# Performance work log

Measured on AMD Instinct MI355X. Metric: run time of the kernel, lower is better.

The kernel has to match this reference:

```python
import jax, jax.numpy as jnp
import numpy as np

HIDDEN = 2048
N_HEADS = 16
N_KV_HEADS = 4
HEAD_DIM = HIDDEN // N_HEADS  # 128
ROPE_THETA = 10000.0
BATCH = 2
SEQ = 2048


def setup_inputs() -> dict:
    key = jax.random.key(0)
    k1, k2, k3, k4, k5 = jax.random.split(key, 5)
    s = 0.02
    return {
        "hidden_states": jax.random.normal(k1, (BATCH, SEQ, HIDDEN), dtype=jnp.float32),
        "attention_mask": jnp.zeros((BATCH, 1, 1, SEQ), dtype=jnp.float32),
        "Wq": jax.random.normal(k2, (HIDDEN, N_HEADS * HEAD_DIM), dtype=jnp.float32) * s,
        "Wk": jax.random.normal(k3, (HIDDEN, N_KV_HEADS * HEAD_DIM), dtype=jnp.float32) * s,
        "Wv": jax.random.normal(k4, (HIDDEN, N_KV_HEADS * HEAD_DIM), dtype=jnp.float32) * s,
        "Wo": jax.random.normal(k5, (N_HEADS * HEAD_DIM, HIDDEN), dtype=jnp.float32) * s,
    }


def _rope_cos_sin(seq_len, dtype):
    inv_freq = 1.0 / (ROPE_THETA ** (jnp.arange(0, HEAD_DIM, 2, dtype=jnp.float32) / HEAD_DIM))
    t = jnp.arange(seq_len, dtype=jnp.float32)
    freqs = t[:, None] * inv_freq[None, :]            # [S, D/2]
    emb = jnp.concatenate([freqs, freqs], axis=-1)    # [S, D]
    cos = jnp.cos(emb)[None, None, :, :].astype(dtype)  # [1,1,S,D]
    sin = jnp.sin(emb)[None, None, :, :].astype(dtype)
    return cos, sin


def _apply_rope(x, cos, sin):
    # x: [B,H,S,D]; faithful to torch code: rotated = cat((-x[...,1::2], x[...,::2]), -1)
    x1 = x[..., ::2]
    x2 = x[..., 1::2]
    rotated = jnp.concatenate([-x2, x1], axis=-1)
    return x * cos + rotated * sin


def reference(hidden_states, attention_mask, Wq, Wk, Wv, Wo):
    B, S, _ = hidden_states.shape
    scale = HEAD_DIM ** -0.5

    q = (hidden_states @ Wq).reshape(B, S, N_HEADS, HEAD_DIM).transpose(0, 2, 1, 3)      # [B,H,S,D]
    k = (hidden_states @ Wk).reshape(B, S, N_KV_HEADS, HEAD_DIM).transpose(0, 2, 1, 3)   # [B,KV,S,D]
    v = (hidden_states @ Wv).reshape(B, S, N_KV_HEADS, HEAD_DIM).transpose(0, 2, 1, 3)

    cos, sin = _rope_cos_sin(S, hidden_states.dtype)
    q = _apply_rope(q, cos, sin)
    k = _apply_rope(k, cos, sin)

    rep = N_HEADS // N_KV_HEADS
    k = jnp.repeat(k, rep, axis=1)  # [B,H,S,D]
    v = jnp.repeat(v, rep, axis=1)

    scores = jnp.einsum("bhqd,bhkd->bhqk", q, k) * scale  # [B,H,S,S]
    causal = jnp.tril(jnp.ones((S, S), dtype=bool))[None, None]
    scores = jnp.where(causal, scores, -jnp.inf)
    scores = scores + attention_mask  # additive float mask, broadcast [B,1,1,S]

    attn = jax.nn.softmax(scores, axis=-1)
    out = jnp.einsum("bhqk,bhkd->bhqd", attn, v)           # [B,H,S,D]
    out = out.transpose(0, 2, 1, 3).reshape(B, S, N_HEADS * HEAD_DIM)
    return out @ Wo
```

## Files before the change

### kernel.cpp

```cpp
#include <hip/hip_runtime.h>
#include <hip/hip_bf16.h>

#define BATCH 2
#define SEQ   2048
#define NH    16
#define NKV   4
#define HD    128
#define KDIM  2048
#define MROWS 4096
#define NQKV  3072

typedef __attribute__((ext_vector_type(8))) short  s16x8;
typedef __attribute__((ext_vector_type(4))) short  s16x4;
typedef __attribute__((ext_vector_type(4))) float  f32x4;
typedef __attribute__((ext_vector_type(8))) __bf16 b16x8;

__device__ __forceinline__ unsigned short f2bf(float f) {
  __hip_bfloat16 h = __float2bfloat16(f);
  return *reinterpret_cast<unsigned short*>(&h);
}
__device__ __forceinline__ float bf2f(unsigned short h) {
  union { unsigned int u; float f; } x; x.u = ((unsigned int)h) << 16;
  return x.f;
}

__device__ __forceinline__ f32x4 MFMA16(s16x8 a, s16x8 b, f32x4 c) {
  return __builtin_amdgcn_mfma_f32_16x16x32_bf16(
      __builtin_bit_cast(b16x8, a), __builtin_bit_cast(b16x8, b), c, 0, 0, 0);
}

__device__ __forceinline__ void gload_lds16(const void* g, void* lds) {
  __builtin_amdgcn_global_load_lds(
      (const __attribute__((address_space(1))) void*)g,
      (__attribute__((address_space(3))) void*)lds, 16, 0, 0);
}

__global__ __launch_bounds__(256) void transpose_convert(
    const float* __restrict__ W, unsigned short* __restrict__ WT, int Kd, int Nd) {
  __shared__ float tile[32][33];
  int n0 = blockIdx.x * 32, k0 = blockIdx.y * 32;
  int tx = threadIdx.x & 31, ty = threadIdx.x >> 5;
#pragma unroll
  for (int i = 0; i < 4; ++i)
    tile[ty + i * 8][tx] = W[(size_t)(k0 + ty + i * 8) * Nd + n0 + tx];
  __syncthreads();
#pragma unroll
  for (int i = 0; i < 4; ++i)
    WT[(size_t)(n0 + ty + i * 8) * Kd + k0 + tx] = f2bf(tile[tx][ty + i * 8]);
}

__global__ __launch_bounds__(256) void conv_bf16(
    const float* __restrict__ X, unsigned short* __restrict__ Y) {
  int i = blockIdx.x * 256 + threadIdx.x;
  const float4 a = ((const float4*)X)[2 * i];
  const float4 b = ((const float4*)X)[2 * i + 1];
  s16x8 o;
  o[0] = (short)f2bf(a.x); o[1] = (short)f2bf(a.y);
  o[2] = (short)f2bf(a.z); o[3] = (short)f2bf(a.w);
  o[4] = (short)f2bf(b.x); o[5] = (short)f2bf(b.y);
  o[6] = (short)f2bf(b.z); o[7] = (short)f2bf(b.w);
  ((s16x8*)Y)[i] = o;
}

__global__ __launch_bounds__(256) void rope_table_kernel(float* __restrict__ tbl) {
  int i = blockIdx.x * 256 + threadIdx.x;
  int s = i >> 6, j = i & 63;
  float inv = powf(10000.0f, -(float)(2 * j) * (1.0f / 128.0f));
  float f = (float)s * inv;
  tbl[2 * i]     = cosf(f);
  tbl[2 * i + 1] = sinf(f);
}

__global__ __launch_bounds__(256) void gemm_qkv(
    const unsigned short* __restrict__ A, const unsigned short* __restrict__ BT,
    unsigned short* __restrict__ Qo, unsigned short* __restrict__ Ko,
    unsigned short* __restrict__ Vo) {
  __shared__ __align__(16) unsigned short la[128][32];
  __shared__ __align__(16) unsigned short lb[128][32];
  int tid = threadIdx.x, lane = tid & 63, w = tid >> 6;
  int m0 = blockIdx.y * 128, n0 = blockIdx.x * 128;
  int wr = (w >> 1) * 64, wc = (w & 1) * 64;
  int fr = lane & 15, kg = (lane >> 4) * 8, rg = (lane >> 4) * 4;
  f32x4 acc[4][4] = {};
  for (int kt = 0; kt < KDIM; kt += 32) {
    __syncthreads();
#pragma unroll
    for (int i = 0; i < 2; ++i) {
      int idx = tid + i * 256;
      int row = idx >> 2, seg = idx & 3;
      gload_lds16(A + (size_t)(m0 + row) * KDIM + kt + seg * 8,
                  (char*)la + (size_t)(i * 256 + w * 64) * 16);
      gload_lds16(BT + (size_t)(n0 + row) * KDIM + kt + seg * 8,
                  (char*)lb + (size_t)(i * 256 + w * 64) * 16);
    }
    __syncthreads();
    s16x8 af[4], bf[4];
#pragma unroll
    for (int mi = 0; mi < 4; ++mi) af[mi] = *(const s16x8*)(&la[wr + mi * 16 + fr][kg]);
#pragma unroll
    for (int ni = 0; ni < 4; ++ni) bf[ni] = *(const s16x8*)(&lb[wc + ni * 16 + fr][kg]);
#pragma unroll
    for (int mi = 0; mi < 4; ++mi)
#pragma unroll
      for (int ni = 0; ni < 4; ++ni) acc[mi][ni] = MFMA16(af[mi], bf[ni], acc[mi][ni]);
  }
  int rbase = m0 + wr + rg;
#pragma unroll
  for (int ni = 0; ni < 4; ++ni) {
    int gn = n0 + wc + ni * 16 + fr;
    if (gn < 2048) {
      int hh = gn >> 7, d = gn & 127;
#pragma unroll
      for (int mi = 0; mi < 4; ++mi)
#pragma unroll
        for (int r = 0; r < 4; ++r) {
          int grow = rbase + mi * 16 + r;
          int bb = grow >> 11, ss = grow & 2047;
          Qo[((size_t)(bb * NH + hh) * SEQ + ss) * HD + d] = f2bf(acc[mi][ni][r]);
        }
    } else if (gn < 2560) {
      int c = gn - 2048, kvh = c >> 7, d = c & 127;
#pragma unroll
      for (int mi = 0; mi < 4; ++mi)
#pragma unroll
        for (int r = 0; r < 4; ++r) {
          int grow = rbase + mi * 16 + r;
          int bb = grow >> 11, ss = grow & 2047;
          Ko[((size_t)(bb * NKV + kvh) * SEQ + ss) * HD + d] = f2bf(acc[mi][ni][r]);
        }
    } else {
      int c = gn - 2560, kvh = c >> 7, d = c & 127;
#pragma unroll
      for (int mi = 0; mi < 4; ++mi) {
        int grow0 = rbase + mi * 16;
        int bb = grow0 >> 11, ss = grow0 & 2047;
        s16x4 pk;
#pragma unroll
        for (int r = 0; r < 4; ++r) pk[r] = (short)f2bf(acc[mi][ni][r]);
        *(s16x4*)(Vo + ((size_t)(bb * NKV + kvh) * HD + d) * SEQ + ss) = pk;
      }
    }
  }
}

__global__ __launch_bounds__(256) void gemm_out(
    const unsigned short* __restrict__ A, const unsigned short* __restrict__ BT,
    float* __restrict__ C) {
  __shared__ __align__(16) unsigned short la[128][32];
  __shared__ __align__(16) unsigned short lb[128][32];
  int tid = threadIdx.x, lane = tid & 63, w = tid >> 6;
  int m0 = blockIdx.y * 128, n0 = blockIdx.x * 128;
  int wr = (w >> 1) * 64, wc = (w & 1) * 64;
  int fr = lane & 15, kg = (lane >> 4) * 8, rg = (lane >> 4) * 4;
  f32x4 acc[4][4] = {};
  for (int kt = 0; kt < KDIM; kt += 32) {
    __syncthreads();
#pragma unroll
    for (int i = 0; i < 2; ++i) {
      int idx = tid + i * 256;
      int row = idx >> 2, seg = idx & 3;
      gload_lds16(A + (size_t)(m0 + row) * KDIM + kt + seg * 8,
                  (char*)la + (size_t)(i * 256 + w * 64) * 16);
      gload_lds16(BT + (size_t)(n0 + row) * KDIM + kt + seg * 8,
                  (char*)lb + (size_t)(i * 256 + w * 64) * 16);
    }
    __syncthreads();
    s16x8 af[4], bf[4];
#pragma unroll
    for (int mi = 0; mi < 4; ++mi) af[mi] = *(const s16x8*)(&la[wr + mi * 16 + fr][kg]);
#pragma unroll
    for (int ni = 0; ni < 4; ++ni) bf[ni] = *(const s16x8*)(&lb[wc + ni * 16 + fr][kg]);
#pragma unroll
    for (int mi = 0; mi < 4; ++mi)
#pragma unroll
      for (int ni = 0; ni < 4; ++ni) acc[mi][ni] = MFMA16(af[mi], bf[ni], acc[mi][ni]);
  }
  int rbase = m0 + wr + rg;
#pragma unroll
  for (int ni = 0; ni < 4; ++ni) {
    int gn = n0 + wc + ni * 16 + fr;
#pragma unroll
    for (int mi = 0; mi < 4; ++mi)
#pragma unroll
      for (int r = 0; r < 4; ++r)
        C[(size_t)(rbase + mi * 16 + r) * 2048 + gn] = acc[mi][ni][r];
  }
}

__global__ __launch_bounds__(256) void rope2(
    unsigned short* __restrict__ X, const float* __restrict__ tbl) {
  __shared__ __align__(16) unsigned short xs[32][136];
  int tid = threadIdx.x;
  size_t r0 = (size_t)blockIdx.x * 32;
#pragma unroll
  for (int i = 0; i < 2; ++i) {
    int idx = tid + i * 256;
    int pr = idx >> 4, seg = idx & 15;
    *(s16x8*)(&xs[pr][seg * 8]) = *(const s16x8*)(X + (r0 + pr) * 128 + seg * 8);
  }
  __syncthreads();
  int pr = tid >> 3, jb = (tid & 7) * 8;
  size_t row = r0 + pr;
  int s = (int)(row & (SEQ - 1));
  s16x8 o0, o1;
#pragma unroll
  for (int j0 = 0; j0 < 8; ++j0) {
    int j = jb + j0;
    float c  = tbl[(s * 64 + j) * 2];
    float sn = tbl[(s * 64 + j) * 2 + 1];
    float xj   = bf2f(xs[pr][j]);
    float xj64 = bf2f(xs[pr][j + 64]);
    float x2j  = bf2f(xs[pr][2 * j]);
    float x2j1 = bf2f(xs[pr][2 * j + 1]);
    o0[j0] = (short)f2bf(xj * c - x2j1 * sn);
    o1[j0] = (short)f2bf(xj64 * c + x2j * sn);
  }
  unsigned short* xp = X + row * 128;
  *(s16x8*)(xp + jb)      = o0;
  *(s16x8*)(xp + 64 + jb) = o1;
}

__global__ __launch_bounds__(256, 2) void attn_fwd(
    const unsigned short* __restrict__ Q, const unsigned short* __restrict__ K,
    const unsigned short* __restrict__ VT, const float* __restrict__ mask,
    unsigned short* __restrict__ O) {
  __shared__ __align__(16) unsigned short kt_[64][136];
  __shared__ __align__(16) unsigned short vt_[128][68];
  __shared__ __align__(16) unsigned short pt_[4][16][36];

  int tid = threadIdx.x, lane = tid & 63, w = tid >> 6;
  int l = blockIdx.x;
  int grp = l & 7, slot = l >> 3;
  int hloc = slot & 3, pair = slot >> 2;
  int b = grp >> 2, kvh = grp & 3, h = kvh * 4 + hloc;
  int fr = lane & 15, g = lane >> 4, kg = g * 8, rg = g * 4;

  const unsigned short* Qb = Q + (size_t)(b * NH + h) * SEQ * HD;
  const unsigned short* Kb = K + (size_t)(b * NKV + kvh) * SEQ * HD;
  const unsigned short* Vb = VT + (size_t)(b * NKV + kvh) * HD * SEQ;
  const float* mb = mask + (size_t)b * SEQ;

  int krow = tid >> 4, kpos = (tid & 15) * 8;
  const float sc2 = 0.12751744584812722f;
  const float L2E = 1.44269504088896f;
  int bS = b * SEQ;

  for (int seg = 0; seg < 2; ++seg) {
    int qt = seg ? pair : 31 - pair;
    int qbase = qt * 64;
    int qw = qbase + w * 16;
    int ntiles = qt + 1;

    s16x8 aq[4];
#pragma unroll
    for (int dc = 0; dc < 4; ++dc)
      aq[dc] = *(const s16x8*)(Qb + (size_t)(qw + fr) * HD + dc * 32 + kg);

    f32x4 oacc[8] = {};
    float m_r = -3e38f, l_r = 0.f;

    s16x8 kreg[4], vreg[4];
#pragma unroll
    for (int i = 0; i < 4; ++i)
      kreg[i] = *(const s16x8*)(Kb + (size_t)(krow + i * 16) * HD + kpos);
#pragma unroll
    for (int i = 0; i < 4; ++i) {
      int c = tid + 256 * i;
      vreg[i] = *(const s16x8*)(Vb + (size_t)(c >> 3) * SEQ + (c & 7) * 8);
    }
#pragma unroll
    for (int i = 0; i < 4; ++i)
      *(s16x8*)(&kt_[krow + i * 16][kpos]) = kreg[i];
    __syncthreads();

    for (int t = 0; t < ntiles; ++t) {
      int kv0 = t * 64;
      bool notlast = (t + 1 < ntiles);
      bool diag = (kv0 + 63 > qw);

#pragma unroll
      for (int i = 0; i < 4; ++i) {
        int c = tid + 256 * i;
        *(s16x8*)(&vt_[c >> 3][(c & 7) * 8]) = vreg[i];
      }
      if (notlast) {
#pragma unroll
        for (int i = 0; i < 4; ++i)
          kreg[i] = *(const s16x8*)(Kb + (size_t)(kv0 + 64 + krow + i * 16) * HD + kpos);
      }

      f32x4 sf[4];
      __builtin_amdgcn_s_setprio(1);
#pragma unroll
      for (int mk = 0; mk < 4; ++mk) {
        s16x8 ak[4];
#pragma unroll
        for (int dc = 0; dc < 4; ++dc)
          ak[dc] = *(const s16x8*)(&kt_[mk * 16 + fr][dc * 32 + kg]);
        sf[mk] = f32x4{0.f, 0.f, 0.f, 0.f};
#pragma unroll
        for (int dc = 0; dc < 4; ++dc)
          sf[mk] = MFMA16(ak[dc], aq[dc], sf[mk]);
      }
      __builtin_amdgcn_s_setprio(0);

#pragma unroll
      for (int mk = 0; mk < 4; ++mk) {
        float4 mv = *(const float4*)(mb + kv0 + mk * 16 + rg);
        float mvr[4] = {mv.x * L2E, mv.y * L2E, mv.z * L2E, mv.w * L2E};
        if (diag) {
#pragma unroll
          for (int r = 0; r < 4; ++r) {
            int kv = kv0 + mk * 16 + rg + r;
            float v = sf[mk][r] * sc2 + mvr[r];
            sf[mk][r] = (kv <= qw + fr) ? v : -3e38f;
          }
        } else {
#pragma unroll
          for (int r = 0; r < 4; ++r)
            sf[mk][r] = sf[mk][r] * sc2 + mvr[r];
        }
      }

      float pm = -3e38f;
#pragma unroll
      for (int mk = 0; mk < 4; ++mk)
#pragma unroll
        for (int r = 0; r < 4; ++r) pm = fmaxf(pm, sf[mk][r]);
      pm = fmaxf(pm, __shfl_xor(pm, 16, 64));
      pm = fmaxf(pm, __shfl_xor(pm, 32, 64));
      if (!__all(pm - m_r <= 8.0f)) {
        float mo = m_r;
        float mn = fmaxf(mo, pm);
        float al = exp2f(mo - mn);
        m_r = mn;
        l_r *= al;
#pragma unroll
        for (int r = 0; r < 4; ++r) {
          float ar = __shfl(al, rg + r, 16);
#pragma unroll
          for (int od = 0; od < 8; ++od) oacc[od][r] *= ar;
        }
      }
      float rs = 0.f;
#pragma unroll
      for (int mk = 0; mk < 4; ++mk)
#pragma unroll
        for (int r = 0; r < 4; ++r) {
          float p = exp2f(sf[mk][r] - m_r);
          sf[mk][r] = p;
          rs += p;
        }
      rs += __shfl_xor(rs, 16, 64);
      rs += __shfl_xor(rs, 32, 64);
      l_r += rs;

      __syncthreads();

      if (notlast) {
#pragma unroll
        for (int i = 0; i < 4; ++i)
          *(s16x8*)(&kt_[krow + i * 16][kpos]) = kreg[i];
#pragma unroll
        for (int i = 0; i < 4; ++i) {
          int c = tid + 256 * i;
          vreg[i] = *(const s16x8*)(Vb + (size_t)(c >> 3) * SEQ + kv0 + 64 + (c & 7) * 8);
        }
      }

#pragma unroll
      for (int kk = 0; kk < 2; ++kk) {
#pragma unroll
        for (int mh = 0; mh < 2; ++mh) {
          int mk = kk * 2 + mh;
          s16x4 pk;
#pragma unroll
          for (int r = 0; r < 4; ++r) pk[r] = (short)f2bf(sf[mk][r]);
          *(s16x4*)(&pt_[w][fr][mh * 16 + rg]) = pk;
        }
        s16x8 ap = *(const s16x8*)(&pt_[w][fr][kg]);
        __builtin_amdgcn_s_setprio(1);
#pragma unroll
        for (int od = 0; od < 8; ++od) {
          s16x8 bv = *(const s16x8*)(&vt_[od * 16 + fr][kk * 32 + kg]);
          oacc[od] = MFMA16(ap, bv, oacc[od]);
        }
        __builtin_amdgcn_s_setprio(0);
      }
      __syncthreads();
    }

    float iv = 1.0f / l_r;
    float ivr[4];
#pragma unroll
    for (int r = 0; r < 4; ++r) ivr[r] = __shfl(iv, rg + r, 16);
#pragma unroll
    for (int r = 0; r < 4; ++r) {
      unsigned short* op = O + (size_t)(bS + qw + rg + r) * 2048 + h * 128 + fr;
#pragma unroll
      for (int od = 0; od < 8; ++od)
        op[od * 16] = f2bf(oacc[od][r] * ivr[r]);
    }
  }
}

extern "C" void kernel_launch(void* const* d_in, const int* in_sizes, int n_in,
                              void* d_out, int out_size, void* d_ws, size_t ws_size,
                              hipStream_t stream) {
  const float* hidden = (const float*)d_in[0];
  const float* mask   = (const float*)d_in[1];
  const float* Wq     = (const float*)d_in[2];
  const float* Wk     = (const float*)d_in[3];
  const float* Wv     = (const float*)d_in[4];
  const float* Wo     = (const float*)d_in[5];
  float* out = (float*)d_out;

  char* ws = (char*)d_ws;
  unsigned short* BT  = (unsigned short*)(ws);
  unsigned short* WoT = (unsigned short*)(ws + 12582912);
  unsigned short* Qb  = (unsigned short*)(ws + 20971520);
  unsigned short* Kb  = (unsigned short*)(ws + 37748736);
  unsigned short* VT  = (unsigned short*)(ws + 41943040);
  unsigned short* AO  = (unsigned short*)(ws + 46137344);
  float*          tbl = (float*)(ws + 62914560);
  unsigned short* Ab  = AO;

  conv_bf16<<<MROWS * KDIM / (256 * 8), 256, 0, stream>>>(hidden, Ab);
  transpose_convert<<<dim3(64, 64), 256, 0, stream>>>(Wq, BT, KDIM, 2048);
  transpose_convert<<<dim3(16, 64), 256, 0, stream>>>(Wk, BT + (size_t)2048 * KDIM, KDIM, 512);
  transpose_convert<<<dim3(16, 64), 256, 0, stream>>>(Wv, BT + (size_t)2560 * KDIM, KDIM, 512);
  transpose_convert<<<dim3(64, 64), 256, 0, stream>>>(Wo, WoT, KDIM, 2048);
  rope_table_kernel<<<512, 256, 0, stream>>>(tbl);

  gemm_qkv<<<dim3(NQKV / 128, MROWS / 128), 256, 0, stream>>>(Ab, BT, Qb, Kb, VT);
  rope2<<<(BATCH * NH * SEQ) / 32, 256, 0, stream>>>(Qb, tbl);
  rope2<<<(BATCH * NKV * SEQ) / 32, 256, 0, stream>>>(Kb, tbl);
  attn_fwd<<<dim3(512), 256, 0, stream>>>(Qb, Kb, VT, mask, AO);
  gemm_out<<<dim3(2048 / 128, MROWS / 128), 256, 0, stream>>>(AO, WoT, out);
}
```

Before: 236.8 us.

## Swizzle GEMM block order, split attention into one q-tile per block, lighter barriers

Both GEMMs now use a 1D grid whose block index is remapped so blocks sharing the same 8-way interleave land on nearby tiles, aiming for better L2 reuse of A/B panels. The attention kernel no longer pairs a long and short q-tile in one block; it launches 1024 blocks with one q-tile each, ordered longest-first, to improve load balance and occupancy. __syncthreads is replaced with an explicit lgkmcnt wait plus s_barrier, and the row-max reduction is written as a tree. Risks include losing the paired balancing and more block launch overhead, and the barrier no longer waits on vector memory counts.

```diff
diff --git a/kernel.cpp b/kernel.cpp
--- a/kernel.cpp
+++ b/kernel.cpp
@@ -14,6 +14,11 @@
 typedef __attribute__((ext_vector_type(4))) short  s16x4;
 typedef __attribute__((ext_vector_type(4))) float  f32x4;
 typedef __attribute__((ext_vector_type(8))) __bf16 b16x8;
+
+#define BARRIER_LDS() do { \
+    asm volatile("s_waitcnt lgkmcnt(0)" ::: "memory"); \
+    __builtin_amdgcn_s_barrier(); \
+  } while (0)
 
 __device__ __forceinline__ unsigned short f2bf(float f) {
   __hip_bfloat16 h = __float2bfloat16(f);
@@ -78,7 +83,10 @@
   __shared__ __align__(16) unsigned short la[128][32];
   __shared__ __align__(16) unsigned short lb[128][32];
   int tid = threadIdx.x, lane = tid & 63, w = tid >> 6;
-  int m0 = blockIdx.y * 128, n0 = blockIdx.x * 128;
+  int lin = blockIdx.x;
+  int swz = (lin & 7) * 96 + (lin >> 3);
+  int bx = swz % 24, by = swz / 24;
+  int m0 = by * 128, n0 = bx * 128;
   int wr = (w >> 1) * 64, wc = (w & 1) * 64;
   int fr = lane & 15, kg = (lane >> 4) * 8, rg = (lane >> 4) * 4;
   f32x4 acc[4][4] = {};
@@ -149,7 +157,10 @@
   __shared__ __align__(16) unsigned short la[128][32];
   __shared__ __align__(16) unsigned short lb[128][32];
   int tid = threadIdx.x, lane = tid & 63, w = tid >> 6;
-  int m0 = blockIdx.y * 128, n0 = blockIdx.x * 128;
+  int lin = blockIdx.x;
+  int swz = (lin & 7) * 64 + (lin >> 3);
+  int bx = swz % 16, by = swz / 16;
+  int m0 = by * 128, n0 = bx * 128;
   int wr = (w >> 1) * 64, wc = (w & 1) * 64;
   int fr = lane & 15, kg = (lane >> 4) * 8, rg = (lane >> 4) * 4;
   f32x4 acc[4][4] = {};
@@ -231,8 +242,10 @@
   int tid = threadIdx.x, lane = tid & 63, w = tid >> 6;
   int l = blockIdx.x;
   int grp = l & 7, slot = l >> 3;
-  int hloc = slot & 3, pair = slot >> 2;
+  int hloc = slot & 3, qt = 31 - (slot >> 2);
   int b = grp >> 2, kvh = grp & 3, h = kvh * 4 + hloc;
+  int qbase = qt * 64;
+  int qw = qbase + w * 16;
   int fr = lane & 15, g = lane >> 4, kg = g * 8, rg = g * 4;
 
   const unsigned short* Qb = Q + (size_t)(b * NH + h) * SEQ * HD;
@@ -244,163 +257,159 @@
   const float sc2 = 0.12751744584812722f;
   const float L2E = 1.44269504088896f;
   int bS = b * SEQ;
-
-  for (int seg = 0; seg < 2; ++seg) {
-    int qt = seg ? pair : 31 - pair;
-    int qbase = qt * 64;
-    int qw = qbase + w * 16;
-    int ntiles = qt + 1;
-
-    s16x8 aq[4];
-#pragma unroll
-    for (int dc = 0; dc < 4; ++dc)
-      aq[dc] = *(const s16x8*)(Qb + (size_t)(qw + fr) * HD + dc * 32 + kg);
-
-    f32x4 oacc[8] = {};
-    float m_r = -3e38f, l_r = 0.f;
-
-    s16x8 kreg[4], vreg[4];
-#pragma unroll
-    for (int i = 0; i < 4; ++i)
-      kreg[i] = *(const s16x8*)(Kb + (size_t)(krow + i * 16) * HD + kpos);
+  int ntiles = qt + 1;
+
+  s16x8 aq[4];
+#pragma unroll
+  for (int dc = 0; dc < 4; ++dc)
+    aq[dc] = *(const s16x8*)(Qb + (size_t)(qw + fr) * HD + dc * 32 + kg);
+
+  f32x4 oacc[8] = {};
+  float m_r = -3e38f, l_r = 0.f;
+
+  s16x8 kreg[4], vreg[4];
+#pragma unroll
+  for (int i = 0; i < 4; ++i)
+    kreg[i] = *(const s16x8*)(Kb + (size_t)(krow + i * 16) * HD + kpos);
+#pragma unroll
+  for (int i = 0; i < 4; ++i) {
+    int c = tid + 256 * i;
+    vreg[i] = *(const s16x8*)(Vb + (size_t)(c >> 3) * SEQ + (c & 7) * 8);
+  }
+#pragma unroll
+  for (int i = 0; i < 4; ++i)
+    *(s16x8*)(&kt_[krow + i * 16][kpos]) = kreg[i];
+  BARRIER_LDS();
+
+  for (int t = 0; t < ntiles; ++t) {
+    int kv0 = t * 64;
+    bool notlast = (t + 1 < ntiles);
+    bool diag = (kv0 + 63 > qw);
+
 #pragma unroll
     for (int i = 0; i < 4; ++i) {
       int c = tid + 256 * i;
-      vreg[i] = *(const s16x8*)(Vb + (size_t)(c >> 3) * SEQ + (c & 7) * 8);
-    }
-#pragma unroll
-    for (int i = 0; i < 4; ++i)
-      *(s16x8*)(&kt_[krow + i * 16][kpos]) = kreg[i];
-    __syncthreads();
-
-    for (int t = 0; t < ntiles; ++t) {
-      int kv0 = t * 64;
-      bool notlast = (t + 1 < ntiles);
-      bool diag = (kv0 + 63 > qw);
-
+      *(s16x8*)(&vt_[c >> 3][(c & 7) * 8]) = vreg[i];
+    }
+    if (notlast) {
+#pragma unroll
+      for (int i = 0; i < 4; ++i)
+        kreg[i] = *(const s16x8*)(Kb + (size_t)(kv0 + 64 + krow + i * 16) * HD + kpos);
+    }
+
+    f32x4 sf[4];
+    __builtin_amdgcn_s_setprio(1);
+#pragma unroll
+    for (int mk = 0; mk < 4; ++mk) {
+      s16x8 ak[4];
+#pragma unroll
+      for (int dc = 0; dc < 4; ++dc)
+        ak[dc] = *(const s16x8*)(&kt_[mk * 16 + fr][dc * 32 + kg]);
+      sf[mk] = f32x4{0.f, 0.f, 0.f, 0.f};
+#pragma unroll
+      for (int dc = 0; dc < 4; ++dc)
+        sf[mk] = MFMA16(ak[dc], aq[dc], sf[mk]);
+    }
+    __builtin_amdgcn_s_setprio(0);
+
+#pragma unroll
+    for (int mk = 0; mk < 4; ++mk) {
+      float4 mv = *(const float4*)(mb + kv0 + mk * 16 + rg);
+      float mvr[4] = {mv.x * L2E, mv.y * L2E, mv.z * L2E, mv.w * L2E};
+      if (diag) {
+#pragma unroll
+        for (int r = 0; r < 4; ++r) {
+          int kv = kv0 + mk * 16 + rg + r;
+          float v = sf[mk][r] * sc2 + mvr[r];
+          sf[mk][r] = (kv <= qw + fr) ? v : -3e38f;
+        }
+      } else {
+#pragma unroll
+        for (int r = 0; r < 4; ++r)
+          sf[mk][r] = sf[mk][r] * sc2 + mvr[r];
+      }
+    }
+
+    float pm01a = fmaxf(sf[0][0], sf[0][1]), pm01b = fmaxf(sf[0][2], sf[0][3]);
+    float pm11a = fmaxf(sf[1][0], sf[1][1]), pm11b = fmaxf(sf[1][2], sf[1][3]);
+    float pm21a = fmaxf(sf[2][0], sf[2][1]), pm21b = fmaxf(sf[2][2], sf[2][3]);
+    float pm31a = fmaxf(sf[3][0], sf[3][1]), pm31b = fmaxf(sf[3][2], sf[3][3]);
+    float pm0 = fmaxf(pm01a, pm01b), pm1 = fmaxf(pm11a, pm11b);
+    float pm2 = fmaxf(pm21a, pm21b), pm3 = fmaxf(pm31a, pm31b);
+    float pm = fmaxf(fmaxf(pm0, pm1), fmaxf(pm2, pm3));
+    pm = fmaxf(pm, __shfl_xor(pm, 16, 64));
+    pm = fmaxf(pm, __shfl_xor(pm, 32, 64));
+    if (!__all(pm - m_r <= 8.0f)) {
+      float mo = m_r;
+      float mn = fmaxf(mo, pm);
+      float al = exp2f(mo - mn);
+      m_r = mn;
+      l_r *= al;
+#pragma unroll
+      for (int r = 0; r < 4; ++r) {
+        float ar = __shfl(al, rg + r, 16);
+#pragma unroll
+        for (int od = 0; od < 8; ++od) oacc[od][r] *= ar;
+      }
+    }
+    float rs = 0.f;
+#pragma unroll
+    for (int mk = 0; mk < 4; ++mk)
+#pragma unroll
+      for (int r = 0; r < 4; ++r) {
+        float ppv = exp2f(sf[mk][r] - m_r);
+        sf[mk][r] = ppv;
+        rs += ppv;
+      }
+    rs += __shfl_xor(rs, 16, 64);
+    rs += __shfl_xor(rs, 32, 64);
+    l_r += rs;
+
+    BARRIER_LDS();
+
+    if (notlast) {
+#pragma unroll
+      for (int i = 0; i < 4; ++i)
+        *(s16x8*)(&kt_[krow + i * 16][kpos]) = kreg[i];
 #pragma unroll
       for (int i = 0; i < 4; ++i) {
         int c = tid + 256 * i;
-        *(s16x8*)(&vt_[c >> 3][(c & 7) * 8]) = vreg[i];
-      }
-      if (notlast) {
-#pragma unroll
-        for (int i = 0; i < 4; ++i)
-          kreg[i] = *(const s16x8*)(Kb + (size_t)(kv0 + 64 + krow + i * 16) * HD + kpos);
-      }
-
-      f32x4 sf[4];
+        vreg[i] = *(const s16x8*)(Vb + (size_t)(c >> 3) * SEQ + kv0 + 64 + (c & 7) * 8);
+      }
+    }
+
+#pragma unroll
+    for (int kk = 0; kk < 2; ++kk) {
+#pragma unroll
+      for (int mh = 0; mh < 2; ++mh) {
+        int mk = kk * 2 + mh;
+        s16x4 pk;
+#pragma unroll
+        for (int r = 0; r < 4; ++r) pk[r] = (short)f2bf(sf[mk][r]);
+        *(s16x4*)(&pt_[w][fr][mh * 16 + rg]) = pk;
+      }
+      s16x8 ap = *(const s16x8*)(&pt_[w][fr][kg]);
       __builtin_amdgcn_s_setprio(1);
 #pragma unroll
-      for (int mk = 0; mk < 4; ++mk) {
-        s16x8 ak[4];
-#pragma unroll
-        for (int dc = 0; dc < 4; ++dc)
-          ak[dc] = *(const s16x8*)(&kt_[mk * 16 + fr][dc * 32 + kg]);
-        sf[mk] = f32x4{0.f, 0.f, 0.f, 0.f};
-#pragma unroll
-        for (int dc = 0; dc < 4; ++dc)
-          sf[mk] = MFMA16(ak[dc], aq[dc], sf[mk]);
+      for (int od = 0; od < 8; ++od) {
+        s16x8 bv = *(const s16x8*)(&vt_[od * 16 + fr][kk * 32 + kg]);
+        oacc[od] = MFMA16(ap, bv, oacc[od]);
       }
       __builtin_amdgcn_s_setprio(0);
-
-#pragma unroll
-      for (int mk = 0; mk < 4; ++mk) {
-        float4 mv = *(const float4*)(mb + kv0 + mk * 16 + rg);
-        float mvr[4] = {mv.x * L2E, mv.y * L2E, mv.z * L2E, mv.w * L2E};
-        if (diag) {
-#pragma unroll
-          for (int r = 0; r < 4; ++r) {
-            int kv = kv0 + mk * 16 + rg + r;
-            float v = sf[mk][r] * sc2 + mvr[r];
-            sf[mk][r] = (kv <= qw + fr) ? v : -3e38f;
-          }
-        } else {
-#pragma unroll
-          for (int r = 0; r < 4; ++r)
-            sf[mk][r] = sf[mk][r] * sc2 + mvr[r];
-        }
-      }
-
-      float pm = -3e38f;
-#pragma unroll
-      for (int mk = 0; mk < 4; ++mk)
-#pragma unroll
-        for (int r = 0; r < 4; ++r) pm = fmaxf(pm, sf[mk][r]);
-      pm = fmaxf(pm, __shfl_xor(pm, 16, 64));
-      pm = fmaxf(pm, __shfl_xor(pm, 32, 64));
-      if (!__all(pm - m_r <= 8.0f)) {
-        float mo = m_r;
-        float mn = fmaxf(mo, pm);
-        float al = exp2f(mo - mn);
-        m_r = mn;
-        l_r *= al;
-#pragma unroll
-        for (int r = 0; r < 4; ++r) {
-          float ar = __shfl(al, rg + r, 16);
-#pragma unroll
-          for (int od = 0; od < 8; ++od) oacc[od][r] *= ar;
-        }
-      }
-      float rs = 0.f;
-#pragma unroll
-      for (int mk = 0; mk < 4; ++mk)
-#pragma unroll
-        for (int r = 0; r < 4; ++r) {
-          float p = exp2f(sf[mk][r] - m_r);
-          sf[mk][r] = p;
-          rs += p;
-        }
-      rs += __shfl_xor(rs, 16, 64);
-      rs += __shfl_xor(rs, 32, 64);
-      l_r += rs;
-
-      __syncthreads();
-
-      if (notlast) {
-#pragma unroll
-        for (int i = 0; i < 4; ++i)
-          *(s16x8*)(&kt_[krow + i * 16][kpos]) = kreg[i];
-#pragma unroll
-        for (int i = 0; i < 4; ++i) {
-          int c = tid + 256 * i;
-          vreg[i] = *(const s16x8*)(Vb + (size_t)(c >> 3) * SEQ + kv0 + 64 + (c & 7) * 8);
-        }
-      }
-
-#pragma unroll
-      for (int kk = 0; kk < 2; ++kk) {
-#pragma unroll
-        for (int mh = 0; mh < 2; ++mh) {
-          int mk = kk * 2 + mh;
-          s16x4 pk;
-#pragma unroll
-          for (int r = 0; r < 4; ++r) pk[r] = (short)f2bf(sf[mk][r]);
-          *(s16x4*)(&pt_[w][fr][mh * 16 + rg]) = pk;
-        }
-        s16x8 ap = *(const s16x8*)(&pt_[w][fr][kg]);
-        __builtin_amdgcn_s_setprio(1);
-#pragma unroll
-        for (int od = 0; od < 8; ++od) {
-          s16x8 bv = *(const s16x8*)(&vt_[od * 16 + fr][kk * 32 + kg]);
-          oacc[od] = MFMA16(ap, bv, oacc[od]);
-        }
-        __builtin_amdgcn_s_setprio(0);
-      }
-      __syncthreads();
-    }
-
-    float iv = 1.0f / l_r;
-    float ivr[4];
-#pragma unroll
-    for (int r = 0; r < 4; ++r) ivr[r] = __shfl(iv, rg + r, 16);
-#pragma unroll
-    for (int r = 0; r < 4; ++r) {
-      unsigned short* op = O + (size_t)(bS + qw + rg + r) * 2048 + h * 128 + fr;
-#pragma unroll
-      for (int od = 0; od < 8; ++od)
-        op[od * 16] = f2bf(oacc[od][r] * ivr[r]);
-    }
+    }
+    BARRIER_LDS();
+  }
+
+  float iv = 1.0f / l_r;
+  float ivr[4];
+#pragma unroll
+  for (int r = 0; r < 4; ++r) ivr[r] = __shfl(iv, rg + r, 16);
+#pragma unroll
+  for (int r = 0; r < 4; ++r) {
+    unsigned short* op = O + (size_t)(bS + qw + rg + r) * 2048 + h * 128 + fr;
+#pragma unroll
+    for (int od = 0; od < 8; ++od)
+      op[od * 16] = f2bf(oacc[od][r] * ivr[r]);
   }
 }
 
@@ -432,9 +441,9 @@
   transpose_convert<<<dim3(64, 64), 256, 0, stream>>>(Wo, WoT, KDIM, 2048);
   rope_table_kernel<<<512, 256, 0, stream>>>(tbl);
 
-  gemm_qkv<<<dim3(NQKV / 128, MROWS / 128), 256, 0, stream>>>(Ab, BT, Qb, Kb, VT);
+  gemm_qkv<<<dim3(768), 256, 0, stream>>>(Ab, BT, Qb, Kb, VT);
   rope2<<<(BATCH * NH * SEQ) / 32, 256, 0, stream>>>(Qb, tbl);
   rope2<<<(BATCH * NKV * SEQ) / 32, 256, 0, stream>>>(Kb, tbl);
-  attn_fwd<<<dim3(512), 256, 0, stream>>>(Qb, Kb, VT, mask, AO);
-  gemm_out<<<dim3(2048 / 128, MROWS / 128), 256, 0, stream>>>(AO, WoT, out);
-}
+  attn_fwd<<<dim3(1024), 256, 0, stream>>>(Qb, Kb, VT, mask, AO);
+  gemm_out<<<dim3(512), 256, 0, stream>>>(AO, WoT, out);
+}
```

Result: faster. 229.3 us (-3.2%).
